# Kernel tuning notes

Hardware: AMD Instinct MI355X
Metric: run time of the kernel (lower is better)

The kernel has to match this reference:

```python
import jax, jax.numpy as jnp
import numpy as np
from jax import lax

V, E, H, K, T = 100000, 256, 512, 16, 4096
START, END = 14, 15
NEG = -10000.0


def setup_inputs() -> dict:
    key = jax.random.key(0)
    ks = jax.random.split(key, 16)
    s = 1.0 / np.sqrt(H)
    u = lambda k, shp: jax.random.uniform(k, shp, jnp.float32, -s, s)
    x = jax.random.randint(ks[0], (1, T), 0, V)
    embed = 0.02 * jax.random.normal(ks[1], (V, E), jnp.float32)
    h0 = jax.random.normal(ks[2], (2, 1, H), jnp.float32)
    c0 = jax.random.normal(ks[3], (2, 1, H), jnp.float32)
    W_ih_f, W_hh_f = u(ks[4], (4 * H, E)), u(ks[5], (4 * H, H))
    b_f = u(ks[6], (4 * H,))
    W_ih_b, W_hh_b = u(ks[7], (4 * H, E)), u(ks[8], (4 * H, H))
    b_b = u(ks[9], (4 * H,))
    fc_w, fc_b = u(ks[10], (K, 2 * H)), u(ks[11], (K,))
    trans = jax.random.normal(ks[12], (K, K), jnp.float32)
    trans = trans.at[START, :].set(NEG).at[:, END].set(NEG)
    return {"x": x, "h0": h0, "c0": c0, "embed": embed,
            "W_ih_f": W_ih_f, "W_hh_f": W_hh_f, "b_f": b_f,
            "W_ih_b": W_ih_b, "W_hh_b": W_hh_b, "b_b": b_b,
            "fc_w": fc_w, "fc_b": fc_b, "transitions": trans}


def _lstm_dir(emb, h0, c0, Wih, Whh, b, reverse):
    # emb: [T, E]; PyTorch gate order i, f, g, o
    def step(carry, xt):
        h, c = carry
        g = xt @ Wih.T + h @ Whh.T + b  # [4H]
        i, f, gg, o = jnp.split(g, 4)
        c = jax.nn.sigmoid(f) * c + jax.nn.sigmoid(i) * jnp.tanh(gg)
        h = jax.nn.sigmoid(o) * jnp.tanh(c)
        return (h, c), h
    _, hs = lax.scan(step, (h0, c0), emb, reverse=reverse)
    return hs  # [T, H]


def reference(x, h0, c0, embed, W_ih_f, W_hh_f, b_f, W_ih_b, W_hh_b, b_b,
              fc_w, fc_b, transitions):
    emb = embed[x[0]]  # [T, E]
    hf = _lstm_dir(emb, h0[0, 0], c0[0, 0], W_ih_f, W_hh_f, b_f, False)
    hb = _lstm_dir(emb, h0[1, 0], c0[1, 0], W_ih_b, W_hh_b, b_b, True)
    lstm_out = jnp.concatenate([hf, hb], axis=-1)  # [T, 2H]
    feats = lstm_out @ fc_w.T + fc_b  # [T, K]

    # Viterbi DP: transitions[next, prev]
    v0 = jnp.full((K,), NEG, jnp.float32).at[START].set(0.0)
    def vit(v, feat):
        sc = v[None, :] + transitions  # [K_next, K_prev]
        return jnp.max(sc, axis=1) + feat, jnp.argmax(sc, axis=1)
    vT, bps = lax.scan(vit, v0, feats)  # bps: [T, K]
    term = vT + transitions[END]
    best = jnp.argmax(term)
    score = term[best]
    def back(tag, bp):
        return bp[tag], tag
    _, path = lax.scan(back, best, bps, reverse=True)  # [T]
    return score, path
```

## Files before the change

kernel.cpp:

```cpp
#include <hip/hip_runtime.h>
#include <hip/hip_bf16.h>

#define T_LEN 4096
#define HID   512
#define EMB   256
#define KTAG  16
#define START_TAG 14
#define END_TAG   15
#define NEGV  (-10000.0f)
#define NWG   64

__device__ __forceinline__ unsigned long long packph(float h, unsigned tag) {
  return ((unsigned long long)tag << 32) | (unsigned long long)__float_as_uint(h);
}
__device__ __forceinline__ unsigned long long ld_pair_agent(const unsigned long long* p) {
  return __hip_atomic_load(p, __ATOMIC_RELAXED, __HIP_MEMORY_SCOPE_AGENT);
}
__device__ __forceinline__ void st_pair_agent(unsigned long long* p, unsigned long long v) {
  __hip_atomic_store(p, v, __ATOMIC_RELAXED, __HIP_MEMORY_SCOPE_AGENT);
}
__device__ __forceinline__ unsigned ptag(unsigned long long v) { return (unsigned)(v >> 32); }

__device__ __forceinline__ float fast_sig(float x) {
  return 1.f / (1.f + __expf(-x));
}
__device__ __forceinline__ float fast_tanh(float x) {
  const float xc = fminf(fmaxf(x, -15.f), 15.f);
  const float e  = __expf(2.f * xc);
  return (e - 1.f) / (e + 1.f);
}

__global__ __launch_bounds__(256, 1) void lstm_kernel(
    const float* __restrict__ Whh_f, const float* __restrict__ Whh_b,
    const float* __restrict__ Wih_f, const float* __restrict__ Wih_b,
    const float* __restrict__ b_f,  const float* __restrict__ b_b,
    const float* __restrict__ h0,   const float* __restrict__ c0,
    const int*   __restrict__ x,    const float* __restrict__ embed,
    unsigned long long* __restrict__ pairs,
    float* __restrict__ hOut)
{
  const int wg   = blockIdx.x;
  const int dir  = wg >> 5;
  const int sl   = wg & 31;
  const int J0   = sl * 16;
  const int tid  = threadIdx.x;
  const int w    = tid >> 6;
  const int l    = tid & 63;
  const int jl   = l & 15;
  const int comp = J0 + jl;
  const int grow = (l >> 4) * HID + comp;

  const float* Whh = dir ? Whh_b : Whh_f;
  const float* Wih = dir ? Wih_b : Wih_f;
  const float* bb  = dir ? b_b  : b_f;

  float wh[128];
  {
    const float* wr = Whh + (size_t)grow * HID + w * 128;
    #pragma unroll
    for (int i = 0; i < 32; ++i)
      *(float4*)&wh[i*4] = *(const float4*)&wr[i*4];
  }
  float we[64];
  {
    const float* wr2 = Wih + (size_t)grow * EMB + w * 64;
    #pragma unroll
    for (int i = 0; i < 16; ++i)
      *(float4*)&we[i*4] = *(const float4*)&wr2[i*4];
  }
  const float bi = bb[comp],        bfg = bb[HID + comp];
  const float bg = bb[2*HID + comp], bo = bb[3*HID + comp];
  float c = c0[dir * HID + comp];

  __shared__ float hl[4][128];
  __shared__ float el[4][64];
  __shared__ float ps[2][4][64];

  unsigned long long* pb = pairs + (size_t)dir * 2 * 512;

  if (w == 0 && l < 16)
    st_pair_agent(&pb[512 + J0 + l], packph(h0[dir*HID + J0 + l], 1u));

  float epf;
  {
    const int tt0 = dir ? (T_LEN - 1) : 0;
    epf = embed[(size_t)x[tt0] * EMB + w * 64 + l];
  }

  unsigned spins = 0;

  for (int t = 0; t < T_LEN; ++t) {
    const int par = t & 1;
    const int tt  = dir ? (T_LEN - 1 - t) : t;

    unsigned long long* psrc = pb + ((par ^ 1) * 512) + w * 128 + 2 * l;
    unsigned long long sp0 = ld_pair_agent(&psrc[0]);
    unsigned long long sp1 = ld_pair_agent(&psrc[1]);

    el[w][l] = epf;
    __builtin_amdgcn_wave_barrier();
    asm volatile("s_waitcnt lgkmcnt(0)" ::: "memory");
    __builtin_amdgcn_sched_barrier(0);

    float acc = 0.f;
    {
      const float* eseg = el[w];
      #pragma unroll
      for (int i = 0; i < 16; ++i) {
        float4 ev = *(const float4*)&eseg[i*4];
        acc += we[i*4+0]*ev.x + we[i*4+1]*ev.y + we[i*4+2]*ev.z + we[i*4+3]*ev.w;
      }
    }

    const unsigned tgt = (unsigned)(t + 1);
    for (;;) {
      const bool f = (ptag(sp0) == tgt) && (ptag(sp1) == tgt);
      if (__all(f)) break;
      if (++spins > 6000000u) break;
      sp0 = ld_pair_agent(&psrc[0]);
      sp1 = ld_pair_agent(&psrc[1]);
    }

    {
      float2 hv2;
      hv2.x = __uint_as_float((unsigned)sp0);
      hv2.y = __uint_as_float((unsigned)sp1);
      *(float2*)&hl[w][2*l] = hv2;
    }
    __builtin_amdgcn_wave_barrier();
    asm volatile("s_waitcnt lgkmcnt(0)" ::: "memory");
    __builtin_amdgcn_sched_barrier(0);

    {
      const float* hseg = hl[w];
      float a0 = 0.f, a1 = 0.f, a2 = 0.f, a3 = 0.f;
      #pragma unroll
      for (int i = 0; i < 8; ++i) {
        float4 h0v = *(const float4*)&hseg[(4*i+0)*4];
        float4 h1v = *(const float4*)&hseg[(4*i+1)*4];
        float4 h2v = *(const float4*)&hseg[(4*i+2)*4];
        float4 h3v = *(const float4*)&hseg[(4*i+3)*4];
        const float* w0 = &wh[(4*i+0)*4];
        const float* w1 = &wh[(4*i+1)*4];
        const float* w2 = &wh[(4*i+2)*4];
        const float* w3 = &wh[(4*i+3)*4];
        a0 += w0[0]*h0v.x + w0[1]*h0v.y + w0[2]*h0v.z + w0[3]*h0v.w;
        a1 += w1[0]*h1v.x + w1[1]*h1v.y + w1[2]*h1v.z + w1[3]*h1v.w;
        a2 += w2[0]*h2v.x + w2[1]*h2v.y + w2[2]*h2v.z + w2[3]*h2v.w;
        a3 += w3[0]*h3v.x + w3[1]*h3v.y + w3[2]*h3v.z + w3[3]*h3v.w;
      }
      acc += (a0 + a1) + (a2 + a3);
    }

    ps[par][w][l] = acc;
    __syncthreads();

    if (w == 0) {
      const float q0 = ps[par][0][l], q1 = ps[par][1][l];
      const float q2 = ps[par][2][l], q3 = ps[par][3][l];
      const float tot = (q0 + q1) + (q2 + q3);
      const float g0 = __shfl(tot, jl);
      const float g1 = __shfl(tot, jl + 16);
      const float g2 = __shfl(tot, jl + 32);
      const float g3 = __shfl(tot, jl + 48);
      const float gi_ = g0 + bi, gf_ = g1 + bfg, gg_ = g2 + bg, go_ = g3 + bo;
      const float si = fast_sig(gi_);
      const float sf = fast_sig(gf_);
      const float so = fast_sig(go_);
      const float cn = sf * c + si * fast_tanh(gg_);
      c = cn;
      const float hv = so * fast_tanh(cn);
      if (l < 16) {
        st_pair_agent(&pb[par * 512 + J0 + l], packph(hv, (unsigned)(t + 2)));
        hOut[((size_t)dir * T_LEN + tt) * HID + J0 + l] = hv;
      }
    }

    if (t + 1 < T_LEN) {
      const int ttn = dir ? (T_LEN - 2 - t) : (t + 1);
      epf = embed[(size_t)x[ttn] * EMB + w * 64 + l];
    }
  }
}

__global__ __launch_bounds__(256) void feats_kernel(
    const float* __restrict__ hOut, const float* __restrict__ fc_w,
    const float* __restrict__ fc_b, float* __restrict__ feats)
{
  const int tid = threadIdx.x;
  const int k   = tid & 15;
  const int tl  = tid >> 4;
  const int t   = blockIdx.x * 16 + tl;
  const float* hf = hOut + (size_t)t * HID;
  const float* hb = hOut + ((size_t)T_LEN + t) * HID;
  const float* wr = fc_w + (size_t)k * (2 * HID);
  float acc = fc_b[k];
  #pragma unroll 4
  for (int j = 0; j < HID; j += 4) {
    float4 hv = *(const float4*)&hf[j];
    float4 wv = *(const float4*)&wr[j];
    acc += hv.x*wv.x + hv.y*wv.y + hv.z*wv.z + hv.w*wv.w;
  }
  #pragma unroll 4
  for (int j = 0; j < HID; j += 4) {
    float4 hv = *(const float4*)&hb[j];
    float4 wv = *(const float4*)&wr[HID + j];
    acc += hv.x*wv.x + hv.y*wv.y + hv.z*wv.z + hv.w*wv.w;
  }
  feats[(size_t)t * KTAG + k] = acc;
}

__global__ __launch_bounds__(256) void viterbi_kernel(
    const float* __restrict__ feats, const float* __restrict__ trans,
    float* __restrict__ out)
{
  __shared__ float fch[256 * KTAG];
  __shared__ unsigned char bps8[T_LEN * 8];
  __shared__ unsigned char ml[64 * 16];
  __shared__ unsigned char rb[64];
  __shared__ int sbest;

  const int tid  = threadIdx.x;
  const int lane = tid & 63;
  const int nxt  = lane >> 2;
  const int pg   = lane & 3;

  float tr[4] = {0.f, 0.f, 0.f, 0.f};
  if (tid < 64) {
    #pragma unroll
    for (int p = 0; p < 4; ++p)
      tr[p] = trans[nxt * KTAG + pg * 4 + p];
  }
  float vlreg = ((lane >> 2) == START_TAG) ? 0.f : NEGV;
  __syncthreads();

  for (int ch = 0; ch < 16; ++ch) {
    const float* src = feats + (size_t)ch * 256 * KTAG;
    #pragma unroll
    for (int i = 0; i < 4; ++i)
      *(float4*)&fch[(i * 256 + tid) * 4] = *(const float4*)&src[(i * 256 + tid) * 4];
    __syncthreads();

    if (tid < 64) {
      const int sbase = pg << 4;
      for (int tl = 0; tl < 256; ++tl) {
        const int t = ch * 256 + tl;
        const float s0 = __shfl(vlreg, sbase);
        const float s1 = __shfl(vlreg, sbase + 4);
        const float s2 = __shfl(vlreg, sbase + 8);
        const float s3 = __shfl(vlreg, sbase + 12);
        float best = s0 + tr[0]; int bp = pg * 4;
        float sc = s1 + tr[1]; if (sc > best) { best = sc; bp = pg * 4 + 1; }
        sc = s2 + tr[2]; if (sc > best) { best = sc; bp = pg * 4 + 2; }
        sc = s3 + tr[3]; if (sc > best) { best = sc; bp = pg * 4 + 3; }
        #pragma unroll
        for (int m = 1; m <= 2; m <<= 1) {
          const float ob = __shfl_xor(best, m);
          const int  obp = __shfl_xor(bp, m);
          if (ob > best || (ob == best && obp < bp)) { best = ob; bp = obp; }
        }
        const int nbp = __shfl(bp, (lane + 4) & 63);
        if (pg == 0 && (nxt & 1) == 0)
          bps8[t * 8 + (nxt >> 1)] = (unsigned char)(bp | (nbp << 4));
        const float fv = fch[tl * KTAG + nxt];
        vlreg = (pg == 0) ? (best + fv) : vlreg;
      }
    }
    __syncthreads();
  }

  if (tid < 64) {
    const float vfin = __shfl(vlreg, (lane & 15) << 2);
    float term = (lane < KTAG) ? (vfin + trans[END_TAG * KTAG + lane]) : -3.0e38f;
    int bt = (lane < KTAG) ? lane : KTAG;
    #pragma unroll
    for (int m = 1; m < 64; m <<= 1) {
      const float ot = __shfl_xor(term, m);
      const int  obt = __shfl_xor(bt, m);
      if (ot > term || (ot == term && obt < bt)) { term = ot; bt = obt; }
    }
    if (lane == 0) { out[0] = term; sbest = bt; }
  }
  __syncthreads();

  if (tid < 64) {
    const int L = lane;
    unsigned char cur[16];
    #pragma unroll
    for (int g = 0; g < 16; ++g) cur[g] = (unsigned char)g;
    for (int i = 63; i >= 0; --i) {
      const int t = L * 64 + i;
      #pragma unroll
      for (int g = 0; g < 16; ++g) {
        const unsigned char cc = cur[g];
        const unsigned char by = bps8[t * 8 + (cc >> 1)];
        cur[g] = (cc & 1) ? (by >> 4) : (by & 15);
      }
    }
    #pragma unroll
    for (int g = 0; g < 16; ++g) ml[L * 16 + g] = cur[g];
  }
  __syncthreads();

  if (tid == 0) {
    int r = sbest;
    rb[63] = (unsigned char)r;
    for (int cix = 62; cix >= 0; --cix) {
      r = ml[(cix + 1) * 16 + r];
      rb[cix] = (unsigned char)r;
    }
  }
  __syncthreads();

  if (tid < 64) {
    const int L = lane;
    int tag = rb[L];
    out[1 + L * 64 + 63] = (float)tag;
    for (int i = 62; i >= 0; --i) {
      const int t = L * 64 + i + 1;
      const unsigned char by = bps8[t * 8 + (tag >> 1)];
      tag = (tag & 1) ? (by >> 4) : (by & 15);
      out[1 + L * 64 + i] = (float)tag;
    }
  }
}

extern "C" void kernel_launch(void* const* d_in, const int* in_sizes, int n_in,
                              void* d_out, int out_size, void* d_ws, size_t ws_size,
                              hipStream_t stream) {
  (void)in_sizes; (void)n_in; (void)out_size; (void)ws_size;
  const int*   x      = (const int*)  d_in[0];
  const float* h0     = (const float*)d_in[1];
  const float* c0     = (const float*)d_in[2];
  const float* embed  = (const float*)d_in[3];
  const float* Wih_f  = (const float*)d_in[4];
  const float* Whh_f  = (const float*)d_in[5];
  const float* b_f    = (const float*)d_in[6];
  const float* Wih_b  = (const float*)d_in[7];
  const float* Whh_b  = (const float*)d_in[8];
  const float* b_b    = (const float*)d_in[9];
  const float* fc_w   = (const float*)d_in[10];
  const float* fc_b   = (const float*)d_in[11];
  const float* trans  = (const float*)d_in[12];
  float* out = (float*)d_out;

  char* ws = (char*)d_ws;
  unsigned long long* pairs = (unsigned long long*)(ws + 0);
  float* feats    = (float*)(ws + 65536);
  float* hOut     = (float*)(ws + (1ull << 20));

  hipMemsetAsync(pairs, 0, 2 * 2 * 512 * sizeof(unsigned long long), stream);

  {
    void* args[] = {
      (void*)&Whh_f, (void*)&Whh_b, (void*)&Wih_f, (void*)&Wih_b,
      (void*)&b_f,   (void*)&b_b,   (void*)&h0,    (void*)&c0,
      (void*)&x,     (void*)&embed, (void*)&pairs, (void*)&hOut
    };
    hipLaunchCooperativeKernel((const void*)lstm_kernel, dim3(NWG), dim3(256),
                               args, 0, stream);
  }

  feats_kernel<<<dim3(T_LEN / 16), 256, 0, stream>>>(hOut, fc_w, fc_b, feats);
  viterbi_kernel<<<dim3(1), 256, 0, stream>>>(feats, trans, out);
}
```

Baseline: 9.696 ms.

## Parallelize Viterbi forward pass via chunked max-plus matrix products and scan

Replaces the single-workgroup sequential Viterbi over 4096 steps with a chunked max-plus approach. Each of 64 blocks first builds a 16x16 max-plus transfer matrix for its 64-step chunk. One block then scans these matrices to get the starting score vector of every chunk, and 64 blocks recompute backpointers in parallel before a final backtrack kernel. This shortens the serial dependency chain at the cost of extra kernel launches and redundant max-plus work.

After: 8.475 ms. -12.6%, faster.

```diff
diff --git a/kernel.cpp b/kernel.cpp
--- a/kernel.cpp
+++ b/kernel.cpp
@@ -210,66 +210,149 @@
   feats[(size_t)t * KTAG + k] = acc;
 }
 
-__global__ __launch_bounds__(256) void viterbi_kernel(
+
+__global__ __launch_bounds__(64) void vit_prod(
     const float* __restrict__ feats, const float* __restrict__ trans,
-    float* __restrict__ out)
-{
-  __shared__ float fch[256 * KTAG];
-  __shared__ unsigned char bps8[T_LEN * 8];
-  __shared__ unsigned char ml[64 * 16];
-  __shared__ unsigned char rb[64];
-  __shared__ int sbest;
-
-  const int tid  = threadIdx.x;
-  const int lane = tid & 63;
+    float* __restrict__ Pg)
+{
+  const int c  = blockIdx.x;
+  const int l  = threadIdx.x;
+  const int n  = l >> 2;
+  const int pg = l & 3;
+  const int t0 = c * 64;
+
+  float tr[16];
+  #pragma unroll
+  for (int k = 0; k < 16; ++k) tr[k] = trans[n * 16 + k];
+
+  __shared__ float PT[2][16][16];
+
+  {
+    const float f0 = feats[t0 * 16 + n];
+    #pragma unroll
+    for (int q = 0; q < 4; ++q)
+      PT[0][4 * pg + q][n] = tr[4 * pg + q] + f0;
+  }
+  __syncthreads();
+
+  int cur = 0;
+  for (int i = 1; i < 64; ++i) {
+    const float fn = feats[(t0 + i) * 16 + n];
+    #pragma unroll
+    for (int q = 0; q < 4; ++q) {
+      const int j = 4 * pg + q;
+      const float* row = PT[cur][j];
+      float m = tr[0] + row[0];
+      #pragma unroll
+      for (int k = 1; k < 16; ++k) m = fmaxf(m, tr[k] + row[k]);
+      PT[cur ^ 1][j][n] = fn + m;
+    }
+    __syncthreads();
+    cur ^= 1;
+  }
+
+  {
+    float4 v;
+    v.x = PT[cur][4 * pg + 0][n];
+    v.y = PT[cur][4 * pg + 1][n];
+    v.z = PT[cur][4 * pg + 2][n];
+    v.w = PT[cur][4 * pg + 3][n];
+    *(float4*)&Pg[(size_t)c * 256 + n * 16 + 4 * pg] = v;
+  }
+}
+
+__global__ __launch_bounds__(64) void vit_scan(
+    const float* __restrict__ Pg, float* __restrict__ vstart)
+{
+  const int l  = threadIdx.x;
+  const int n  = l >> 2;
+  const int pg = l & 3;
+
+  float v4[4];
+  #pragma unroll
+  for (int p = 0; p < 4; ++p) v4[p] = (4 * pg + p == START_TAG) ? 0.f : NEGV;
+
+  float4 P4 = *(const float4*)&Pg[(size_t)0 * 256 + n * 16 + 4 * pg];
+
+  for (int c = 0; c < 64; ++c) {
+    if (n == 0)
+      *(float4*)&vstart[c * 16 + 4 * pg] = *(float4*)v4;
+
+    float4 Pn;
+    if (c + 1 < 64)
+      Pn = *(const float4*)&Pg[(size_t)(c + 1) * 256 + n * 16 + 4 * pg];
+
+    float part = P4.x + v4[0];
+    part = fmaxf(part, P4.y + v4[1]);
+    part = fmaxf(part, P4.z + v4[2]);
+    part = fmaxf(part, P4.w + v4[3]);
+    part = fmaxf(part, __shfl_xor(part, 1));
+    part = fmaxf(part, __shfl_xor(part, 2));
+    #pragma unroll
+    for (int p = 0; p < 4; ++p)
+      v4[p] = __shfl(part, (4 * pg + p) << 2);
+
+    P4 = Pn;
+  }
+}
+
+__global__ __launch_bounds__(64) void vit_rec(
+    const float* __restrict__ feats, const float* __restrict__ trans,
+    const float* __restrict__ vstart,
+    unsigned long long* __restrict__ bpsg,
+    unsigned char* __restrict__ gmaps,
+    int* __restrict__ sbest_g, float* __restrict__ out)
+{
+  const int c    = blockIdx.x;
+  const int lane = threadIdx.x;
   const int nxt  = lane >> 2;
   const int pg   = lane & 3;
 
-  float tr[4] = {0.f, 0.f, 0.f, 0.f};
-  if (tid < 64) {
-    #pragma unroll
-    for (int p = 0; p < 4; ++p)
-      tr[p] = trans[nxt * KTAG + pg * 4 + p];
-  }
-  float vlreg = ((lane >> 2) == START_TAG) ? 0.f : NEGV;
+  __shared__ float fch[64 * KTAG];
+  __shared__ unsigned char bps8[64 * 8];
+
+  {
+    const float* src = feats + (size_t)c * 64 * KTAG + lane * KTAG;
+    #pragma unroll
+    for (int i = 0; i < 4; ++i)
+      *(float4*)&fch[lane * KTAG + i * 4] = *(const float4*)&src[i * 4];
+  }
+
+  float tr[4];
+  #pragma unroll
+  for (int p = 0; p < 4; ++p)
+    tr[p] = trans[nxt * KTAG + pg * 4 + p];
+
+  float vlreg = vstart[c * 16 + (lane >> 2)];
   __syncthreads();
 
-  for (int ch = 0; ch < 16; ++ch) {
-    const float* src = feats + (size_t)ch * 256 * KTAG;
-    #pragma unroll
-    for (int i = 0; i < 4; ++i)
-      *(float4*)&fch[(i * 256 + tid) * 4] = *(const float4*)&src[(i * 256 + tid) * 4];
-    __syncthreads();
-
-    if (tid < 64) {
-      const int sbase = pg << 4;
-      for (int tl = 0; tl < 256; ++tl) {
-        const int t = ch * 256 + tl;
-        const float s0 = __shfl(vlreg, sbase);
-        const float s1 = __shfl(vlreg, sbase + 4);
-        const float s2 = __shfl(vlreg, sbase + 8);
-        const float s3 = __shfl(vlreg, sbase + 12);
-        float best = s0 + tr[0]; int bp = pg * 4;
-        float sc = s1 + tr[1]; if (sc > best) { best = sc; bp = pg * 4 + 1; }
-        sc = s2 + tr[2]; if (sc > best) { best = sc; bp = pg * 4 + 2; }
-        sc = s3 + tr[3]; if (sc > best) { best = sc; bp = pg * 4 + 3; }
-        #pragma unroll
-        for (int m = 1; m <= 2; m <<= 1) {
-          const float ob = __shfl_xor(best, m);
-          const int  obp = __shfl_xor(bp, m);
-          if (ob > best || (ob == best && obp < bp)) { best = ob; bp = obp; }
-        }
-        const int nbp = __shfl(bp, (lane + 4) & 63);
-        if (pg == 0 && (nxt & 1) == 0)
-          bps8[t * 8 + (nxt >> 1)] = (unsigned char)(bp | (nbp << 4));
-        const float fv = fch[tl * KTAG + nxt];
-        vlreg = (pg == 0) ? (best + fv) : vlreg;
+  {
+    const int sbase = pg << 4;
+    for (int tl2 = 0; tl2 < 64; ++tl2) {
+      const float s0 = __shfl(vlreg, sbase);
+      const float s1 = __shfl(vlreg, sbase + 4);
+      const float s2 = __shfl(vlreg, sbase + 8);
+      const float s3 = __shfl(vlreg, sbase + 12);
+      float best = s0 + tr[0]; int bp = pg * 4;
+      float sc = s1 + tr[1]; if (sc > best) { best = sc; bp = pg * 4 + 1; }
+      sc = s2 + tr[2]; if (sc > best) { best = sc; bp = pg * 4 + 2; }
+      sc = s3 + tr[3]; if (sc > best) { best = sc; bp = pg * 4 + 3; }
+      #pragma unroll
+      for (int m = 1; m <= 2; m <<= 1) {
+        const float ob = __shfl_xor(best, m);
+        const int  obp = __shfl_xor(bp, m);
+        if (ob > best || (ob == best && obp < bp)) { best = ob; bp = obp; }
       }
-    }
-    __syncthreads();
-  }
-
-  if (tid < 64) {
+      const int nbp = __shfl(bp, (lane + 4) & 63);
+      if (pg == 0 && (nxt & 1) == 0)
+        bps8[tl2 * 8 + (nxt >> 1)] = (unsigned char)(bp | (nbp << 4));
+      const float fv = fch[tl2 * KTAG + nxt];
+      vlreg = (pg == 0) ? (best + fv) : vlreg;
+    }
+  }
+  __syncthreads();
+
+  if (c == 63) {
     const float vfin = __shfl(vlreg, (lane & 15) << 2);
     float term = (lane < KTAG) ? (vfin + trans[END_TAG * KTAG + lane]) : -3.0e38f;
     int bt = (lane < KTAG) ? lane : KTAG;
@@ -279,31 +362,47 @@
       const int  obt = __shfl_xor(bt, m);
       if (ot > term || (ot == term && obt < bt)) { term = ot; bt = obt; }
     }
-    if (lane == 0) { out[0] = term; sbest = bt; }
+    if (lane == 0) { out[0] = term; *sbest_g = bt; }
+  }
+
+  if (lane < 16) {
+    int cc = lane;
+    for (int i = 63; i >= 0; --i) {
+      const unsigned char by = bps8[i * 8 + (cc >> 1)];
+      cc = (cc & 1) ? (by >> 4) : (by & 15);
+    }
+    gmaps[c * 16 + lane] = (unsigned char)cc;
+  }
+
+  bpsg[(size_t)c * 64 + lane] = ((const unsigned long long*)bps8)[lane];
+}
+
+__global__ __launch_bounds__(256) void vit_back(
+    const unsigned long long* __restrict__ bpsg,
+    const unsigned char* __restrict__ gmaps,
+    const int* __restrict__ sbest_g, float* __restrict__ out)
+{
+  __shared__ unsigned char bps8[T_LEN * 8];
+  __shared__ unsigned char ml[64 * 16];
+  __shared__ unsigned char rb[64];
+
+  const int tid = threadIdx.x;
+
+  {
+    unsigned long long* d = (unsigned long long*)bps8;
+    #pragma unroll
+    for (int i = 0; i < 16; ++i)
+      d[tid * 16 + i] = bpsg[tid * 16 + i];
+  }
+  if (tid < 64) {
+    #pragma unroll
+    for (int g = 0; g < 16; ++g)
+      ml[tid * 16 + g] = gmaps[tid * 16 + g];
   }
   __syncthreads();
 
-  if (tid < 64) {
-    const int L = lane;
-    unsigned char cur[16];
-    #pragma unroll
-    for (int g = 0; g < 16; ++g) cur[g] = (unsigned char)g;
-    for (int i = 63; i >= 0; --i) {
-      const int t = L * 64 + i;
-      #pragma unroll
-      for (int g = 0; g < 16; ++g) {
-        const unsigned char cc = cur[g];
-        const unsigned char by = bps8[t * 8 + (cc >> 1)];
-        cur[g] = (cc & 1) ? (by >> 4) : (by & 15);
-      }
-    }
-    #pragma unroll
-    for (int g = 0; g < 16; ++g) ml[L * 16 + g] = cur[g];
-  }
-  __syncthreads();
-
   if (tid == 0) {
-    int r = sbest;
+    int r = *sbest_g;
     rb[63] = (unsigned char)r;
     for (int cix = 62; cix >= 0; --cix) {
       r = ml[(cix + 1) * 16 + r];
@@ -313,7 +412,7 @@
   __syncthreads();
 
   if (tid < 64) {
-    const int L = lane;
+    const int L = tid;
     int tag = rb[L];
     out[1 + L * 64 + 63] = (float)tag;
     for (int i = 62; i >= 0; --i) {
@@ -345,9 +444,14 @@
   float* out = (float*)d_out;
 
   char* ws = (char*)d_ws;
-  unsigned long long* pairs = (unsigned long long*)(ws + 0);
-  float* feats    = (float*)(ws + 65536);
-  float* hOut     = (float*)(ws + (1ull << 20));
+  unsigned long long* pairs  = (unsigned long long*)(ws + 0);
+  float* feats               = (float*)(ws + 65536);
+  float* Pg                  = (float*)(ws + 327680);
+  float* vstart              = (float*)(ws + 393216);
+  unsigned char* gmaps       = (unsigned char*)(ws + 397312);
+  int* sbest_g               = (int*)(ws + 398336);
+  unsigned long long* bpsg   = (unsigned long long*)(ws + 399360);
+  float* hOut                = (float*)(ws + (1ull << 20));
 
   hipMemsetAsync(pairs, 0, 2 * 2 * 512 * sizeof(unsigned long long), stream);
 
@@ -362,5 +466,9 @@
   }
 
   feats_kernel<<<dim3(T_LEN / 16), 256, 0, stream>>>(hOut, fc_w, fc_b, feats);
-  viterbi_kernel<<<dim3(1), 256, 0, stream>>>(feats, trans, out);
-}
+  vit_prod<<<dim3(64), 64, 0, stream>>>(feats, trans, Pg);
+  vit_scan<<<dim3(1), 64, 0, stream>>>(Pg, vstart);
+  vit_rec <<<dim3(64), 64, 0, stream>>>(feats, trans, vstart, bpsg, gmaps,
+                                        sbest_g, out);
+  vit_back<<<dim3(1), 256, 0, stream>>>(bpsg, gmaps, sbest_g, out);
+}
```
